# Optimization experiments

Hardware: AMD Instinct MI355X
Metric: run time of the kernel (lower is better)

## Reference

```python
import jax, jax.numpy as jnp
import numpy as np


def setup_inputs() -> dict:
    key = jax.random.key(0)
    ks = jax.random.split(key, 8)
    B, A = 2048, 64
    STATE, ACT = 5, 4
    d_in = STATE + ACT  # 9
    x = jax.random.normal(ks[0], (B, STATE), dtype=jnp.float32)
    actions = jax.random.normal(ks[1], (A, ACT), dtype=jnp.float32)
    def lin(k, fin, fout):
        return jax.random.normal(k, (fin, fout), dtype=jnp.float32) / np.sqrt(fin)
    W1 = lin(ks[2], d_in, 128); b1 = jnp.zeros((128,), jnp.float32)
    W2 = lin(ks[3], 128, 1024); b2 = jnp.zeros((1024,), jnp.float32)
    W3 = lin(ks[4], 1024, 1024); b3 = jnp.zeros((1024,), jnp.float32)
    W4 = lin(ks[5], 1024, 128); b4 = jnp.zeros((128,), jnp.float32)
    W5 = lin(ks[6], 128, 1); b5 = jnp.zeros((1,), jnp.float32)
    return {"x": x, "actions": actions,
            "W1": W1, "b1": b1, "W2": W2, "b2": b2, "W3": W3, "b3": b3,
            "W4": W4, "b4": b4, "W5": W5, "b5": b5}


def reference(x, actions, W1, b1, W2, b2, W3, b3, W4, b4, W5, b5):
    # x: [B,5] states; actions: [A,4] candidate actions.
    # Equivalent to the original's per-sample per-action loop: evaluate the
    # 5-layer Tanh MLP on concat(state, action) for every (sample, action) pair.
    B = x.shape[0]
    A = actions.shape[0]
    s = jnp.broadcast_to(x[:, None, :], (B, A, x.shape[1]))
    a = jnp.broadcast_to(actions[None, :, :], (B, A, actions.shape[1]))
    inp = jnp.concatenate([s, a], axis=-1)  # [B,A,9]
    h = jnp.tanh(inp @ W1 + b1)
    h = jnp.tanh(h @ W2 + b2)
    h = jnp.tanh(h @ W3 + b3)
    h = jnp.tanh(h @ W4 + b4)
    values = (h @ W5 + b5)[..., 0]  # [B,A]
    best = jnp.argmax(values, axis=1)  # [B]
    max_value_action = actions[best]  # [B,4]
    return (max_value_action, values)
```

## Files before the change

kernel.cpp:

```cpp
#include <hip/hip_runtime.h>
#include <math.h>


typedef short bf16x8 __attribute__((ext_vector_type(8)));
typedef float f32x4 __attribute__((ext_vector_type(4)));
typedef float f32x16 __attribute__((ext_vector_type(16)));

__device__ __host__ inline unsigned short f2bf(float f) {
    union { float f; unsigned u; } v; v.f = f;
    unsigned r = v.u + 0x7fff + ((v.u >> 16) & 1);
    return (unsigned short)(r >> 16);
}
__device__ inline float bf2f(unsigned short b) {
    union { unsigned u; float f; } v; v.u = ((unsigned)b) << 16;
    return v.f;
}
__device__ inline float fast_tanh(float x) {
    float e = __expf(2.0f * x);
    return 1.0f - 2.0f * __builtin_amdgcn_rcpf(e + 1.0f);
}

#define DELTA 0.025f
#define WL_CAP 4096

struct WLE { unsigned long long mask; unsigned s; unsigned pad; };

#define HSWZ(row, b) ((b) ^ (((row) & 15) << 4))

__global__ __launch_bounds__(256) void pack_w16(const float* __restrict__ src,
                                                unsigned short* __restrict__ dst,
                                                int K, int N) {
    int tid = blockIdx.x * 256 + threadIdx.x;
    int blob = tid >> 6, lane = tid & 63;
    int bpn = K >> 5;
    int nblob = (N >> 4) * bpn;
    if (blob >= nblob) return;
    int nt = blob / bpn, kt = blob % bpn;
    int n = nt * 16 + (lane & 15);
    int kbase = kt * 32 + ((lane >> 4) & 3) * 8;
    bf16x8 v;
    #pragma unroll
    for (int e = 0; e < 8; ++e) v[e] = (short)f2bf(src[(size_t)(kbase + e) * N + n]);
    *(bf16x8*)&dst[(size_t)blob * 512 + lane * 8] = v;
}
__global__ __launch_bounds__(256) void pack_w32(const float* __restrict__ src,
                                                unsigned short* __restrict__ dst,
                                                int K, int N) {
    int tid = blockIdx.x * 256 + threadIdx.x;
    int blob = tid >> 6, lane = tid & 63;
    int bpn = K >> 4;
    int nblob = (N >> 5) * bpn;
    if (blob >= nblob) return;
    int nt = blob / bpn, kt = blob % bpn;
    int n = nt * 32 + (lane & 31);
    int kbase = kt * 16 + (lane >> 5) * 8;
    bf16x8 v;
    #pragma unroll
    for (int e = 0; e < 8; ++e) v[e] = (short)f2bf(src[(size_t)(kbase + e) * N + n]);
    *(bf16x8*)&dst[(size_t)blob * 512 + lane * 8] = v;
}

__global__ __launch_bounds__(1024, 4) void qnet_mfma(
    const float* __restrict__ x, const float* __restrict__ actions,
    const float* __restrict__ W1, const float* __restrict__ b1,
    const float* __restrict__ b2, const float* __restrict__ b3,
    const float* __restrict__ b4,
    const float* __restrict__ W5, const float* __restrict__ b5,
    const unsigned short* __restrict__ W2p,
    const unsigned short* __restrict__ W3p,
    const unsigned short* __restrict__ W4p,
    float* __restrict__ values)
{
    __shared__ unsigned short h2[64 * 1024];
    __shared__ unsigned short hc[64 * 128];

    const int t = threadIdx.x;
    const int lane = t & 63;
    const int wave = t >> 6;
    const int p0 = blockIdx.x * 64;
    const int kb16 = (lane >> 4) * 16;
    const int kb32 = (lane >> 5) * 16;

    {
        int r = t >> 4;
        int c0 = (t & 15) * 8;
        const float* xs = &x[blockIdx.x * 5];
        const float* as = &actions[r * 4];
        float in[9] = { xs[0], xs[1], xs[2], xs[3], xs[4], as[0], as[1], as[2], as[3] };
        #pragma unroll
        for (int j = 0; j < 8; ++j) {
            int c = c0 + j;
            float acc = b1[c];
            #pragma unroll
            for (int k = 0; k < 9; ++k) acc += in[k] * W1[k * 128 + c];
            *(unsigned short*)((char*)hc + r * 256 + HSWZ(r, c * 2)) = f2bf(fast_tanh(acc));
        }
    }
    __syncthreads();

    {
        bf16x8 Af[4][4];
        #pragma unroll
        for (int rt = 0; rt < 4; ++rt)
            #pragma unroll
            for (int ks = 0; ks < 4; ++ks) {
                int row = rt * 16 + (lane & 15);
                Af[rt][ks] = *(const bf16x8*)((const char*)hc + row * 256 + HSWZ(row, ks * 64 + kb16));
            }
        #pragma unroll
        for (int j = 0; j < 4; ++j) {
            int nT = wave * 4 + j;
            float bv = b2[nT * 16 + (lane & 15)];
            f32x4 acc0 = (f32x4){ bv, bv, bv, bv };
            f32x4 acc1 = acc0, acc2 = acc0, acc3v = acc0;
            #pragma unroll
            for (int ks = 0; ks < 4; ++ks) {
                bf16x8 b = *(const bf16x8*)&W2p[((size_t)(nT * 4 + ks)) * 512 + lane * 8];
                acc0 = __builtin_amdgcn_mfma_f32_16x16x32_bf16(Af[0][ks], b, acc0, 0, 0, 0);
                acc1 = __builtin_amdgcn_mfma_f32_16x16x32_bf16(Af[1][ks], b, acc1, 0, 0, 0);
                acc2 = __builtin_amdgcn_mfma_f32_16x16x32_bf16(Af[2][ks], b, acc2, 0, 0, 0);
                acc3v = __builtin_amdgcn_mfma_f32_16x16x32_bf16(Af[3][ks], b, acc3v, 0, 0, 0);
            }
            int n = nT * 16 + (lane & 15);
            #pragma unroll
            for (int rr = 0; rr < 4; ++rr) {
                int m0 = (lane >> 4) * 4 + rr;
                *(unsigned short*)((char*)h2 + (m0 +  0) * 2048 + HSWZ(m0 +  0, n * 2)) = f2bf(fast_tanh(acc0[rr]));
                *(unsigned short*)((char*)h2 + (m0 + 16) * 2048 + HSWZ(m0 + 16, n * 2)) = f2bf(fast_tanh(acc1[rr]));
                *(unsigned short*)((char*)h2 + (m0 + 32) * 2048 + HSWZ(m0 + 32, n * 2)) = f2bf(fast_tanh(acc2[rr]));
                *(unsigned short*)((char*)h2 + (m0 + 48) * 2048 + HSWZ(m0 + 48, n * 2)) = f2bf(fast_tanh(acc3v[rr]));
            }
        }
    }
    __syncthreads();

    f32x16 a00, a01, a10, a11;
    {
        float bv0 = b3[wave * 64 + (lane & 31)];
        float bv1 = b3[wave * 64 + 32 + (lane & 31)];
        #pragma unroll
        for (int i = 0; i < 16; ++i) { a00[i] = bv0; a10[i] = bv0; a01[i] = bv1; a11[i] = bv1; }
    }
    const int r0 = lane & 31, r1 = 32 + (lane & 31);
    {
        const unsigned short* bbase = &W3p[((size_t)(wave * 2) * 64) * 512 + lane * 8];
        #pragma unroll 2
        for (int kt = 0; kt < 64; ++kt) {
            bf16x8 A0 = *(const bf16x8*)((const char*)h2 + r0 * 2048 + HSWZ(r0, kt * 32 + kb32));
            bf16x8 A1 = *(const bf16x8*)((const char*)h2 + r1 * 2048 + HSWZ(r1, kt * 32 + kb32));
            bf16x8 B0 = *(const bf16x8*)(bbase + (size_t)kt * 512);
            bf16x8 B1 = *(const bf16x8*)(bbase + (size_t)(64 + kt) * 512);
            a00 = __builtin_amdgcn_mfma_f32_32x32x16_bf16(A0, B0, a00, 0, 0, 0);
            a10 = __builtin_amdgcn_mfma_f32_32x32x16_bf16(A1, B0, a10, 0, 0, 0);
            a01 = __builtin_amdgcn_mfma_f32_32x32x16_bf16(A0, B1, a01, 0, 0, 0);
            a11 = __builtin_amdgcn_mfma_f32_32x32x16_bf16(A1, B1, a11, 0, 0, 0);
        }
    }
    __syncthreads();

    {
        int c0l = wave * 64 + (lane & 31);
        #pragma unroll
        for (int r = 0; r < 16; ++r) {
            int row = (r & 3) + 8 * (r >> 2) + 4 * (lane >> 5);
            int rowB = row + 32;
            *(unsigned short*)((char*)h2 + row  * 2048 + HSWZ(row,  c0l * 2)) = f2bf(fast_tanh(a00[r]));
            *(unsigned short*)((char*)h2 + rowB * 2048 + HSWZ(rowB, c0l * 2)) = f2bf(fast_tanh(a10[r]));
            *(unsigned short*)((char*)h2 + row  * 2048 + HSWZ(row,  (c0l + 32) * 2)) = f2bf(fast_tanh(a01[r]));
            *(unsigned short*)((char*)h2 + rowB * 2048 + HSWZ(rowB, (c0l + 32) * 2)) = f2bf(fast_tanh(a11[r]));
        }
    }
    __syncthreads();

    {
        const int ct = wave & 7, rtp = wave >> 3;
        const int rowA = rtp * 32 + (lane & 15);
        const int rowB = rowA + 16;
        float bv = b4[ct * 16 + (lane & 15)];
        f32x4 acc4a = (f32x4){ bv, bv, bv, bv };
        f32x4 acc4b = acc4a;
        #pragma unroll 4
        for (int k32 = 0; k32 < 32; ++k32) {
            bf16x8 B = *(const bf16x8*)&W4p[((size_t)(ct * 32 + k32)) * 512 + lane * 8];
            bf16x8 aA = *(const bf16x8*)((const char*)h2 + rowA * 2048 + HSWZ(rowA, k32 * 64 + kb16));
            bf16x8 aB = *(const bf16x8*)((const char*)h2 + rowB * 2048 + HSWZ(rowB, k32 * 64 + kb16));
            acc4a = __builtin_amdgcn_mfma_f32_16x16x32_bf16(aA, B, acc4a, 0, 0, 0);
            acc4b = __builtin_amdgcn_mfma_f32_16x16x32_bf16(aB, B, acc4b, 0, 0, 0);
        }
        int n = ct * 16 + (lane & 15);
        #pragma unroll
        for (int rr = 0; rr < 4; ++rr) {
            int mA = rtp * 32 + (lane >> 4) * 4 + rr;
            int mB = mA + 16;
            *(unsigned short*)((char*)hc + mA * 256 + HSWZ(mA, n * 2)) = f2bf(fast_tanh(acc4a[rr]));
            *(unsigned short*)((char*)hc + mB * 256 + HSWZ(mB, n * 2)) = f2bf(fast_tanh(acc4b[rr]));
        }
    }
    __syncthreads();

    {
        int r = t >> 4, g = t & 15;
        float part = 0.0f;
        #pragma unroll
        for (int j = 0; j < 8; ++j) {
            int cidx = g * 8 + j;
            unsigned short hb = *(const unsigned short*)((const char*)hc + r * 256 + HSWZ(r, cidx * 2));
            part += bf2f(hb) * W5[cidx];
        }
        part += __shfl_down(part, 8);
        part += __shfl_down(part, 4);
        part += __shfl_down(part, 2);
        part += __shfl_down(part, 1);
        if (g == 0) values[p0 + r] = part + b5[0];
    }
}

__global__ void wl_init(unsigned* wl_cnt) {
    if (threadIdx.x == 0 && blockIdx.x == 0) *wl_cnt = 0u;
}

__global__ __launch_bounds__(256) void scan_argmax(
    const float* __restrict__ values, const float* __restrict__ actions,
    float* __restrict__ out_actions, unsigned* __restrict__ wl_cnt,
    WLE* __restrict__ wl)
{
    int wave = threadIdx.x >> 6, lane = threadIdx.x & 63;
    int s = blockIdx.x * 4 + wave;
    float myv = values[s * 64 + lane];
    float v = myv; int idx = lane;
    #pragma unroll
    for (int off = 32; off; off >>= 1) {
        float ov = __shfl_down(v, off);
        int oi = __shfl_down(idx, off);
        if (ov > v || (ov == v && oi < idx)) { v = ov; idx = oi; }
    }
    float vm = __shfl(v, 0);
    int best = __shfl(idx, 0);
    unsigned long long mask = __ballot(myv >= vm - DELTA);
    if (lane == 0 && __popcll(mask) > 1) {
        unsigned slot = atomicAdd(wl_cnt, 1u);
        if (slot < WL_CAP) { wl[slot].mask = mask; wl[slot].s = (unsigned)s; }
    }
    if (lane < 4) out_actions[s * 4 + lane] = actions[best * 4 + lane];
}

__global__ __launch_bounds__(256) void fixup_eval(
    const float* __restrict__ x, const float* __restrict__ actions,
    const float* __restrict__ W1, const float* __restrict__ b1,
    const float* __restrict__ W2, const float* __restrict__ b2,
    const float* __restrict__ W3, const float* __restrict__ b3,
    const float* __restrict__ W4, const float* __restrict__ b4,
    const float* __restrict__ W5, const float* __restrict__ b5,
    const unsigned* __restrict__ wl_cnt, const WLE* __restrict__ wl,
    float* __restrict__ out_actions)
{
    __shared__ float h1s[8][128];
    __shared__ float h2s[8][1024];
    __shared__ float h3s[8][1024];
    __shared__ float h4s[8][128];
    __shared__ float ain[8][4];
    __shared__ float xs[5];
    __shared__ int cand[64];
    __shared__ int ncand;
    __shared__ float vals[8];
    __shared__ float bestv; __shared__ int besti;

    const int t = threadIdx.x;
    int n = (int)*wl_cnt;
    if (n > WL_CAP) n = WL_CAP;
    for (int e = blockIdx.x; e < n; e += gridDim.x) {
        unsigned long long mask = wl[e].mask;
        int s = (int)wl[e].s;
        if (t == 0) {
            int nn = 0; unsigned long long m2 = mask;
            while (m2) { cand[nn++] = __ffsll(m2) - 1; m2 &= m2 - 1; }
            ncand = nn; bestv = -1e30f; besti = 0;
        }
        if (t < 5) xs[t] = x[s * 5 + t];
        __syncthreads();
        const int NC = ncand;
        for (int g = 0; g < NC; g += 8) {
            if (t < 32) {
                int rr = t >> 2;
                int src = (g + rr < NC) ? cand[g + rr] : cand[g];
                ain[rr][t & 3] = actions[src * 4 + (t & 3)];
            }
            __syncthreads();
            {
                int r = t >> 5, cb = (t & 31) * 4;
                #pragma unroll
                for (int j = 0; j < 4; ++j) {
                    int c = cb + j;
                    float acc = b1[c];
                    #pragma unroll
                    for (int k = 0; k < 5; ++k) acc += xs[k] * W1[k * 128 + c];
                    #pragma unroll
                    for (int k = 0; k < 4; ++k) acc += ain[r][k] * W1[(5 + k) * 128 + c];
                    h1s[r][c] = tanhf(acc);
                }
            }
            __syncthreads();
            {
                int cb = t * 4;
                float acc[8][4];
                float4 bv = *(const float4*)&b2[cb];
                #pragma unroll
                for (int r = 0; r < 8; ++r) { acc[r][0]=bv.x; acc[r][1]=bv.y; acc[r][2]=bv.z; acc[r][3]=bv.w; }
                for (int k = 0; k < 128; ++k) {
                    float4 w = *(const float4*)&W2[k * 1024 + cb];
                    #pragma unroll
                    for (int r = 0; r < 8; ++r) {
                        float hv = h1s[r][k];
                        acc[r][0] += hv * w.x; acc[r][1] += hv * w.y;
                        acc[r][2] += hv * w.z; acc[r][3] += hv * w.w;
                    }
                }
                #pragma unroll
                for (int r = 0; r < 8; ++r) {
                    h2s[r][cb+0] = tanhf(acc[r][0]); h2s[r][cb+1] = tanhf(acc[r][1]);
                    h2s[r][cb+2] = tanhf(acc[r][2]); h2s[r][cb+3] = tanhf(acc[r][3]);
                }
            }
            __syncthreads();
            {
                int cb = t * 4;
                float acc[8][4];
                float4 bv = *(const float4*)&b3[cb];
                #pragma unroll
                for (int r = 0; r < 8; ++r) { acc[r][0]=bv.x; acc[r][1]=bv.y; acc[r][2]=bv.z; acc[r][3]=bv.w; }
                for (int k = 0; k < 1024; ++k) {
                    float4 w = *(const float4*)&W3[k * 1024 + cb];
                    #pragma unroll
                    for (int r = 0; r < 8; ++r) {
                        float hv = h2s[r][k];
                        acc[r][0] += hv * w.x; acc[r][1] += hv * w.y;
                        acc[r][2] += hv * w.z; acc[r][3] += hv * w.w;
                    }
                }
                #pragma unroll
                for (int r = 0; r < 8; ++r) {
                    h3s[r][cb+0] = tanhf(acc[r][0]); h3s[r][cb+1] = tanhf(acc[r][1]);
                    h3s[r][cb+2] = tanhf(acc[r][2]); h3s[r][cb+3] = tanhf(acc[r][3]);
                }
            }
            __syncthreads();
            {
                int r = t >> 5, cb = (t & 31) * 4;
                float acc[4];
                float4 bv = *(const float4*)&b4[cb];
                acc[0]=bv.x; acc[1]=bv.y; acc[2]=bv.z; acc[3]=bv.w;
                for (int k = 0; k < 1024; ++k) {
                    float4 w = *(const float4*)&W4[k * 128 + cb];
                    float hv = h3s[r][k];
                    acc[0] += hv * w.x; acc[1] += hv * w.y; acc[2] += hv * w.z; acc[3] += hv * w.w;
                }
                h4s[r][cb+0] = tanhf(acc[0]); h4s[r][cb+1] = tanhf(acc[1]);
                h4s[r][cb+2] = tanhf(acc[2]); h4s[r][cb+3] = tanhf(acc[3]);
            }
            __syncthreads();
            if (t < 8) {
                float acc = b5[0];
                for (int k = 0; k < 128; ++k) acc += h4s[t][k] * W5[k];
                vals[t] = acc;
            }
            __syncthreads();
            if (t == 0) {
                int lim = (NC - g < 8) ? (NC - g) : 8;
                for (int i = 0; i < lim; ++i)
                    if (vals[i] > bestv) { bestv = vals[i]; besti = cand[g + i]; }
            }
            __syncthreads();
        }
        if (t < 4) out_actions[s * 4 + t] = actions[besti * 4 + t];
        __syncthreads();
    }
}

#define TR 16
__global__ __launch_bounds__(256) void qnet_fused(
    const float* __restrict__ x, const float* __restrict__ actions,
    const float* __restrict__ W1, const float* __restrict__ b1,
    const float* __restrict__ W2, const float* __restrict__ b2,
    const float* __restrict__ W3, const float* __restrict__ b3,
    const float* __restrict__ W4, const float* __restrict__ b4,
    const float* __restrict__ W5, const float* __restrict__ b5,
    float* __restrict__ values)
{
    __shared__ float h_small[TR][128];
    __shared__ float hA[TR][1024];
    __shared__ float hB[TR][1024];
    const int t = threadIdx.x;
    const int p0 = blockIdx.x * TR;
    for (int i = t; i < TR * 128; i += 256) {
        int r = i >> 7, c = i & 127;
        int p = p0 + r;
        int bidx = p >> 6, aidx = p & 63;
        float acc = b1[c];
        for (int k = 0; k < 5; ++k) acc += x[bidx * 5 + k] * W1[k * 128 + c];
        for (int k = 0; k < 4; ++k) acc += actions[aidx * 4 + k] * W1[(5 + k) * 128 + c];
        h_small[r][c] = tanhf(acc);
    }
    __syncthreads();
    {
        const int c0 = t * 4;
        float4 bias = *(const float4*)&b2[c0];
        float acc[TR][4];
        for (int r = 0; r < TR; ++r) { acc[r][0]=bias.x; acc[r][1]=bias.y; acc[r][2]=bias.z; acc[r][3]=bias.w; }
        for (int k = 0; k < 128; k += 4) {
            float4 w0 = *(const float4*)&W2[(k+0)*1024+c0];
            float4 w1 = *(const float4*)&W2[(k+1)*1024+c0];
            float4 w2 = *(const float4*)&W2[(k+2)*1024+c0];
            float4 w3 = *(const float4*)&W2[(k+3)*1024+c0];
            for (int r = 0; r < TR; ++r) {
                float4 hv = *(const float4*)&h_small[r][k];
                acc[r][0] += hv.x*w0.x + hv.y*w1.x + hv.z*w2.x + hv.w*w3.x;
                acc[r][1] += hv.x*w0.y + hv.y*w1.y + hv.z*w2.y + hv.w*w3.y;
                acc[r][2] += hv.x*w0.z + hv.y*w1.z + hv.z*w2.z + hv.w*w3.z;
                acc[r][3] += hv.x*w0.w + hv.y*w1.w + hv.z*w2.w + hv.w*w3.w;
            }
        }
        for (int r = 0; r < TR; ++r) {
            hA[r][c0+0]=tanhf(acc[r][0]); hA[r][c0+1]=tanhf(acc[r][1]);
            hA[r][c0+2]=tanhf(acc[r][2]); hA[r][c0+3]=tanhf(acc[r][3]);
        }
    }
    __syncthreads();
    {
        const int c0 = t * 4;
        float4 bias = *(const float4*)&b3[c0];
        float acc[TR][4];
        for (int r = 0; r < TR; ++r) { acc[r][0]=bias.x; acc[r][1]=bias.y; acc[r][2]=bias.z; acc[r][3]=bias.w; }
        for (int k = 0; k < 1024; k += 4) {
            float4 w0 = *(const float4*)&W3[(k+0)*1024+c0];
            float4 w1 = *(const float4*)&W3[(k+1)*1024+c0];
            float4 w2 = *(const float4*)&W3[(k+2)*1024+c0];
            float4 w3 = *(const float4*)&W3[(k+3)*1024+c0];
            for (int r = 0; r < TR; ++r) {
                float4 hv = *(const float4*)&hA[r][k];
                acc[r][0] += hv.x*w0.x + hv.y*w1.x + hv.z*w2.x + hv.w*w3.x;
                acc[r][1] += hv.x*w0.y + hv.y*w1.y + hv.z*w2.y + hv.w*w3.y;
                acc[r][2] += hv.x*w0.z + hv.y*w1.z + hv.z*w2.z + hv.w*w3.z;
                acc[r][3] += hv.x*w0.w + hv.y*w1.w + hv.z*w2.w + hv.w*w3.w;
            }
        }
        for (int r = 0; r < TR; ++r) {
            hB[r][c0+0]=tanhf(acc[r][0]); hB[r][c0+1]=tanhf(acc[r][1]);
            hB[r][c0+2]=tanhf(acc[r][2]); hB[r][c0+3]=tanhf(acc[r][3]);
        }
    }
    __syncthreads();
    {
        const int c = t & 127;
        const int rh = t >> 7;
        float acc[8];
        float bias = b4[c];
        for (int r = 0; r < 8; ++r) acc[r] = bias;
        for (int k = 0; k < 1024; k += 4) {
            float w0 = W4[(k+0)*128+c], w1 = W4[(k+1)*128+c];
            float w2 = W4[(k+2)*128+c], w3 = W4[(k+3)*128+c];
            for (int r = 0; r < 8; ++r) {
                float4 hv = *(const float4*)&hB[rh*8+r][k];
                acc[r] += hv.x*w0 + hv.y*w1 + hv.z*w2 + hv.w*w3;
            }
        }
        for (int r = 0; r < 8; ++r) h_small[rh*8+r][c] = tanhf(acc[r]);
    }
    __syncthreads();
    if (t < TR) {
        float acc = b5[0];
        for (int k = 0; k < 128; k += 4) {
            float4 hv = *(const float4*)&h_small[t][k];
            float4 wv = *(const float4*)&W5[k];
            acc += hv.x*wv.x + hv.y*wv.y + hv.z*wv.z + hv.w*wv.w;
        }
        values[p0 + t] = acc;
    }
}

__global__ __launch_bounds__(256) void argmax_gather(
    const float* __restrict__ values, const float* __restrict__ actions,
    float* __restrict__ out_actions)
{
    const int wave = threadIdx.x >> 6;
    const int lane = threadIdx.x & 63;
    const int state = blockIdx.x * (blockDim.x >> 6) + wave;
    float v = values[state * 64 + lane];
    int idx = lane;
    for (int off = 32; off; off >>= 1) {
        float ov = __shfl_down(v, off);
        int oi = __shfl_down(idx, off);
        if (ov > v || (ov == v && oi < idx)) { v = ov; idx = oi; }
    }
    idx = __shfl(idx, 0);
    if (lane < 4) out_actions[state * 4 + lane] = actions[idx * 4 + lane];
}

extern "C" void kernel_launch(void* const* d_in, const int* in_sizes, int n_in,
                              void* d_out, int out_size, void* d_ws, size_t ws_size,
                              hipStream_t stream) {
    const float* x       = (const float*)d_in[0];
    const float* actions = (const float*)d_in[1];
    const float* W1 = (const float*)d_in[2];  const float* b1 = (const float*)d_in[3];
    const float* W2 = (const float*)d_in[4];  const float* b2 = (const float*)d_in[5];
    const float* W3 = (const float*)d_in[6];  const float* b3 = (const float*)d_in[7];
    const float* W4 = (const float*)d_in[8];  const float* b4 = (const float*)d_in[9];
    const float* W5 = (const float*)d_in[10]; const float* b5 = (const float*)d_in[11];

    float* out_actions = (float*)d_out;
    float* values      = (float*)d_out + 2048 * 4;

    const size_t nW2 = 128 * 1024, nW3 = 1024 * 1024, nW4 = 1024 * 128;
    const size_t wbytes = (nW2 + nW3 + nW4) * sizeof(unsigned short);
    const size_t need = wbytes + 16 + (size_t)WL_CAP * sizeof(WLE);

    if (ws_size >= need) {
        unsigned short* W2p = (unsigned short*)d_ws;
        unsigned short* W3p = W2p + nW2;
        unsigned short* W4p = W3p + nW3;
        unsigned* wl_cnt = (unsigned*)((char*)d_ws + wbytes);
        WLE* wl = (WLE*)((char*)d_ws + wbytes + 16);

        pack_w16<<<(int)((nW2 / 8 + 255) / 256), 256, 0, stream>>>(W2, W2p, 128, 1024);
        pack_w32<<<(int)((nW3 / 8 + 255) / 256), 256, 0, stream>>>(W3, W3p, 1024, 1024);
        pack_w16<<<(int)((nW4 / 8 + 255) / 256), 256, 0, stream>>>(W4, W4p, 1024, 128);
        wl_init<<<1, 64, 0, stream>>>(wl_cnt);
        qnet_mfma<<<2048, 1024, 0, stream>>>(x, actions, W1, b1, b2, b3, b4, W5, b5,
                                             W2p, W3p, W4p, values);
        scan_argmax<<<512, 256, 0, stream>>>(values, actions, out_actions, wl_cnt, wl);
        fixup_eval<<<512, 256, 0, stream>>>(x, actions, W1, b1, W2, b2, W3, b3,
                                            W4, b4, W5, b5, wl_cnt, wl, out_actions);
    } else {
        qnet_fused<<<2048 * 64 / TR, 256, 0, stream>>>(x, actions, W1, b1, W2, b2, W3, b3,
                                                       W4, b4, W5, b5, values);
        argmax_gather<<<2048 / 4, 256, 0, stream>>>(values, actions, out_actions);
    }
}
```

Measured before the change: 626.4 us.

## Chunk layer-2 into double-buffered LDS stages and merge weight-packing launches

```diff
diff --git a/kernel.cpp b/kernel.cpp
--- a/kernel.cpp
+++ b/kernel.cpp
@@ -27,37 +27,40 @@
 
 #define HSWZ(row, b) ((b) ^ (((row) & 15) << 4))
 
-__global__ __launch_bounds__(256) void pack_w16(const float* __restrict__ src,
-                                                unsigned short* __restrict__ dst,
-                                                int K, int N) {
+__global__ __launch_bounds__(256) void pack_all(
+    const float* __restrict__ W2, const float* __restrict__ W3, const float* __restrict__ W4,
+    unsigned short* __restrict__ W2p, unsigned short* __restrict__ W3p,
+    unsigned short* __restrict__ W4p, unsigned* __restrict__ wl_cnt)
+{
     int tid = blockIdx.x * 256 + threadIdx.x;
+    if (tid == 0) *wl_cnt = 0u;
     int blob = tid >> 6, lane = tid & 63;
-    int bpn = K >> 5;
-    int nblob = (N >> 4) * bpn;
-    if (blob >= nblob) return;
-    int nt = blob / bpn, kt = blob % bpn;
-    int n = nt * 16 + (lane & 15);
-    int kbase = kt * 32 + ((lane >> 4) & 3) * 8;
+    if (blob >= 2560) return;
     bf16x8 v;
-    #pragma unroll
-    for (int e = 0; e < 8; ++e) v[e] = (short)f2bf(src[(size_t)(kbase + e) * N + n]);
-    *(bf16x8*)&dst[(size_t)blob * 512 + lane * 8] = v;
-}
-__global__ __launch_bounds__(256) void pack_w32(const float* __restrict__ src,
-                                                unsigned short* __restrict__ dst,
-                                                int K, int N) {
-    int tid = blockIdx.x * 256 + threadIdx.x;
-    int blob = tid >> 6, lane = tid & 63;
-    int bpn = K >> 4;
-    int nblob = (N >> 5) * bpn;
-    if (blob >= nblob) return;
-    int nt = blob / bpn, kt = blob % bpn;
-    int n = nt * 32 + (lane & 31);
-    int kbase = kt * 16 + (lane >> 5) * 8;
-    bf16x8 v;
-    #pragma unroll
-    for (int e = 0; e < 8; ++e) v[e] = (short)f2bf(src[(size_t)(kbase + e) * N + n]);
-    *(bf16x8*)&dst[(size_t)blob * 512 + lane * 8] = v;
+    if (blob < 256) {
+        int nt = blob >> 2, kt = blob & 3;
+        int n = nt * 16 + (lane & 15);
+        int kbase = kt * 32 + ((lane >> 4) & 3) * 8;
+        #pragma unroll
+        for (int e = 0; e < 8; ++e) v[e] = (short)f2bf(W2[(size_t)(kbase + e) * 1024 + n]);
+        *(bf16x8*)&W2p[(size_t)blob * 512 + lane * 8] = v;
+    } else if (blob < 2304) {
+        int lb = blob - 256;
+        int nt = lb >> 6, kt = lb & 63;
+        int n = nt * 32 + (lane & 31);
+        int kbase = kt * 16 + (lane >> 5) * 8;
+        #pragma unroll
+        for (int e = 0; e < 8; ++e) v[e] = (short)f2bf(W3[(size_t)(kbase + e) * 1024 + n]);
+        *(bf16x8*)&W3p[(size_t)lb * 512 + lane * 8] = v;
+    } else {
+        int lb = blob - 2304;
+        int nt = lb >> 5, kt = lb & 31;
+        int n = nt * 16 + (lane & 15);
+        int kbase = kt * 32 + ((lane >> 4) & 3) * 8;
+        #pragma unroll
+        for (int e = 0; e < 8; ++e) v[e] = (short)f2bf(W4[(size_t)(kbase + e) * 128 + n]);
+        *(bf16x8*)&W4p[(size_t)lb * 512 + lane * 8] = v;
+    }
 }
 
 __global__ __launch_bounds__(1024, 4) void qnet_mfma(
@@ -71,7 +74,7 @@
     const unsigned short* __restrict__ W4p,
     float* __restrict__ values)
 {
-    __shared__ unsigned short h2[64 * 1024];
+    __shared__ unsigned short h2b[2][64 * 256];
     __shared__ unsigned short hc[64 * 128];
 
     const int t = threadIdx.x;
@@ -98,41 +101,34 @@
     }
     __syncthreads();
 
-    {
-        bf16x8 Af[4][4];
-        #pragma unroll
-        for (int rt = 0; rt < 4; ++rt)
-            #pragma unroll
-            for (int ks = 0; ks < 4; ++ks) {
-                int row = rt * 16 + (lane & 15);
-                Af[rt][ks] = *(const bf16x8*)((const char*)hc + row * 256 + HSWZ(row, ks * 64 + kb16));
-            }
-        #pragma unroll
-        for (int j = 0; j < 4; ++j) {
-            int nT = wave * 4 + j;
-            float bv = b2[nT * 16 + (lane & 15)];
-            f32x4 acc0 = (f32x4){ bv, bv, bv, bv };
-            f32x4 acc1 = acc0, acc2 = acc0, acc3v = acc0;
-            #pragma unroll
-            for (int ks = 0; ks < 4; ++ks) {
-                bf16x8 b = *(const bf16x8*)&W2p[((size_t)(nT * 4 + ks)) * 512 + lane * 8];
-                acc0 = __builtin_amdgcn_mfma_f32_16x16x32_bf16(Af[0][ks], b, acc0, 0, 0, 0);
-                acc1 = __builtin_amdgcn_mfma_f32_16x16x32_bf16(Af[1][ks], b, acc1, 0, 0, 0);
-                acc2 = __builtin_amdgcn_mfma_f32_16x16x32_bf16(Af[2][ks], b, acc2, 0, 0, 0);
-                acc3v = __builtin_amdgcn_mfma_f32_16x16x32_bf16(Af[3][ks], b, acc3v, 0, 0, 0);
-            }
-            int n = nT * 16 + (lane & 15);
-            #pragma unroll
-            for (int rr = 0; rr < 4; ++rr) {
-                int m0 = (lane >> 4) * 4 + rr;
-                *(unsigned short*)((char*)h2 + (m0 +  0) * 2048 + HSWZ(m0 +  0, n * 2)) = f2bf(fast_tanh(acc0[rr]));
-                *(unsigned short*)((char*)h2 + (m0 + 16) * 2048 + HSWZ(m0 + 16, n * 2)) = f2bf(fast_tanh(acc1[rr]));
-                *(unsigned short*)((char*)h2 + (m0 + 32) * 2048 + HSWZ(m0 + 32, n * 2)) = f2bf(fast_tanh(acc2[rr]));
-                *(unsigned short*)((char*)h2 + (m0 + 48) * 2048 + HSWZ(m0 + 48, n * 2)) = f2bf(fast_tanh(acc3v[rr]));
-            }
-        }
-    }
-    __syncthreads();
+    auto layer2_chunk = [&](int c, int buf) {
+        int nT = c * 16 + wave;
+        float bv = b2[nT * 16 + (lane & 15)];
+        f32x4 acc0 = (f32x4){ bv, bv, bv, bv };
+        f32x4 acc1 = acc0, acc2 = acc0, acc3v = acc0;
+        #pragma unroll
+        for (int ks = 0; ks < 4; ++ks) {
+            bf16x8 b = *(const bf16x8*)&W2p[((size_t)(nT * 4 + ks)) * 512 + lane * 8];
+            bf16x8 a0 = *(const bf16x8*)((const char*)hc + ( 0 + (lane & 15)) * 256 + HSWZ((lane & 15),      ks * 64 + kb16));
+            bf16x8 a1 = *(const bf16x8*)((const char*)hc + (16 + (lane & 15)) * 256 + HSWZ(16 + (lane & 15), ks * 64 + kb16));
+            bf16x8 a2 = *(const bf16x8*)((const char*)hc + (32 + (lane & 15)) * 256 + HSWZ(32 + (lane & 15), ks * 64 + kb16));
+            bf16x8 a3 = *(const bf16x8*)((const char*)hc + (48 + (lane & 15)) * 256 + HSWZ(48 + (lane & 15), ks * 64 + kb16));
+            acc0 = __builtin_amdgcn_mfma_f32_16x16x32_bf16(a0, b, acc0, 0, 0, 0);
+            acc1 = __builtin_amdgcn_mfma_f32_16x16x32_bf16(a1, b, acc1, 0, 0, 0);
+            acc2 = __builtin_amdgcn_mfma_f32_16x16x32_bf16(a2, b, acc2, 0, 0, 0);
+            acc3v = __builtin_amdgcn_mfma_f32_16x16x32_bf16(a3, b, acc3v, 0, 0, 0);
+        }
+        int lc = wave * 16 + (lane & 15);
+        char* bufp = (char*)&h2b[buf][0];
+        #pragma unroll
+        for (int rr = 0; rr < 4; ++rr) {
+            int m0 = (lane >> 4) * 4 + rr;
+            *(unsigned short*)(bufp + (m0 +  0) * 512 + HSWZ(m0 +  0, lc * 2)) = f2bf(fast_tanh(acc0[rr]));
+            *(unsigned short*)(bufp + (m0 + 16) * 512 + HSWZ(m0 + 16, lc * 2)) = f2bf(fast_tanh(acc1[rr]));
+            *(unsigned short*)(bufp + (m0 + 32) * 512 + HSWZ(m0 + 32, lc * 2)) = f2bf(fast_tanh(acc2[rr]));
+            *(unsigned short*)(bufp + (m0 + 48) * 512 + HSWZ(m0 + 48, lc * 2)) = f2bf(fast_tanh(acc3v[rr]));
+        }
+    };
 
     f32x16 a00, a01, a10, a11;
     {
@@ -141,62 +137,61 @@
         #pragma unroll
         for (int i = 0; i < 16; ++i) { a00[i] = bv0; a10[i] = bv0; a01[i] = bv1; a11[i] = bv1; }
     }
+
+    layer2_chunk(0, 0);
+    __syncthreads();
+
     const int r0 = lane & 31, r1 = 32 + (lane & 31);
-    {
-        const unsigned short* bbase = &W3p[((size_t)(wave * 2) * 64) * 512 + lane * 8];
+    for (int c = 0; c < 4; ++c) {
+        if (c < 3) layer2_chunk(c + 1, (c + 1) & 1);
+        const char* buf = (const char*)&h2b[c & 1][0];
+        const unsigned short* bb = &W3p[((size_t)((wave * 2) * 64 + c * 16)) * 512 + lane * 8];
         #pragma unroll 2
-        for (int kt = 0; kt < 64; ++kt) {
-            bf16x8 A0 = *(const bf16x8*)((const char*)h2 + r0 * 2048 + HSWZ(r0, kt * 32 + kb32));
-            bf16x8 A1 = *(const bf16x8*)((const char*)h2 + r1 * 2048 + HSWZ(r1, kt * 32 + kb32));
-            bf16x8 B0 = *(const bf16x8*)(bbase + (size_t)kt * 512);
-            bf16x8 B1 = *(const bf16x8*)(bbase + (size_t)(64 + kt) * 512);
+        for (int kt = 0; kt < 16; ++kt) {
+            bf16x8 A0 = *(const bf16x8*)(buf + r0 * 512 + HSWZ(r0, kt * 32 + kb32));
+            bf16x8 A1 = *(const bf16x8*)(buf + r1 * 512 + HSWZ(r1, kt * 32 + kb32));
+            bf16x8 B0 = *(const bf16x8*)(bb + (size_t)kt * 512);
+            bf16x8 B1 = *(const bf16x8*)(bb + (size_t)(64 + kt) * 512);
             a00 = __builtin_amdgcn_mfma_f32_32x32x16_bf16(A0, B0, a00, 0, 0, 0);
             a10 = __builtin_amdgcn_mfma_f32_32x32x16_bf16(A1, B0, a10, 0, 0, 0);
             a01 = __builtin_amdgcn_mfma_f32_32x32x16_bf16(A0, B1, a01, 0, 0, 0);
             a11 = __builtin_amdgcn_mfma_f32_32x32x16_bf16(A1, B1, a11, 0, 0, 0);
         }
-    }
-    __syncthreads();
-
-    {
-        int c0l = wave * 64 + (lane & 31);
+        __syncthreads();
+    }
+
+    char* stage = (char*)&h2b[0][0];
+    const int ct = wave & 7, rtp = wave >> 3;
+    const int c0l = wave * 64 + (lane & 31);
+    const float bv4 = b4[ct * 16 + (lane & 15)];
+
+    #pragma unroll
+    for (int h = 0; h < 2; ++h) {
         #pragma unroll
         for (int r = 0; r < 16; ++r) {
             int row = (r & 3) + 8 * (r >> 2) + 4 * (lane >> 5);
-            int rowB = row + 32;
-            *(unsigned short*)((char*)h2 + row  * 2048 + HSWZ(row,  c0l * 2)) = f2bf(fast_tanh(a00[r]));
-            *(unsigned short*)((char*)h2 + rowB * 2048 + HSWZ(rowB, c0l * 2)) = f2bf(fast_tanh(a10[r]));
-            *(unsigned short*)((char*)h2 + row  * 2048 + HSWZ(row,  (c0l + 32) * 2)) = f2bf(fast_tanh(a01[r]));
-            *(unsigned short*)((char*)h2 + rowB * 2048 + HSWZ(rowB, (c0l + 32) * 2)) = f2bf(fast_tanh(a11[r]));
-        }
-    }
-    __syncthreads();
-
-    {
-        const int ct = wave & 7, rtp = wave >> 3;
-        const int rowA = rtp * 32 + (lane & 15);
-        const int rowB = rowA + 16;
-        float bv = b4[ct * 16 + (lane & 15)];
-        f32x4 acc4a = (f32x4){ bv, bv, bv, bv };
-        f32x4 acc4b = acc4a;
+            float vlo = h ? a10[r] : a00[r];
+            float vhi = h ? a11[r] : a01[r];
+            *(unsigned short*)(stage + row * 2048 + HSWZ(row, c0l * 2)) = f2bf(fast_tanh(vlo));
+            *(unsigned short*)(stage + row * 2048 + HSWZ(row, (c0l + 32) * 2)) = f2bf(fast_tanh(vhi));
+        }
+        __syncthreads();
+        f32x4 acc4 = (f32x4){ bv4, bv4, bv4, bv4 };
+        const int rowL = rtp * 16 + (lane & 15);
         #pragma unroll 4
         for (int k32 = 0; k32 < 32; ++k32) {
             bf16x8 B = *(const bf16x8*)&W4p[((size_t)(ct * 32 + k32)) * 512 + lane * 8];
-            bf16x8 aA = *(const bf16x8*)((const char*)h2 + rowA * 2048 + HSWZ(rowA, k32 * 64 + kb16));
-            bf16x8 aB = *(const bf16x8*)((const char*)h2 + rowB * 2048 + HSWZ(rowB, k32 * 64 + kb16));
-            acc4a = __builtin_amdgcn_mfma_f32_16x16x32_bf16(aA, B, acc4a, 0, 0, 0);
-            acc4b = __builtin_amdgcn_mfma_f32_16x16x32_bf16(aB, B, acc4b, 0, 0, 0);
+            bf16x8 a = *(const bf16x8*)(stage + rowL * 2048 + HSWZ(rowL, k32 * 64 + kb16));
+            acc4 = __builtin_amdgcn_mfma_f32_16x16x32_bf16(a, B, acc4, 0, 0, 0);
         }
         int n = ct * 16 + (lane & 15);
         #pragma unroll
         for (int rr = 0; rr < 4; ++rr) {
-            int mA = rtp * 32 + (lane >> 4) * 4 + rr;
-            int mB = mA + 16;
-            *(unsigned short*)((char*)hc + mA * 256 + HSWZ(mA, n * 2)) = f2bf(fast_tanh(acc4a[rr]));
-            *(unsigned short*)((char*)hc + mB * 256 + HSWZ(mB, n * 2)) = f2bf(fast_tanh(acc4b[rr]));
-        }
-    }
-    __syncthreads();
+            int m = h * 32 + rtp * 16 + (lane >> 4) * 4 + rr;
+            *(unsigned short*)((char*)hc + m * 256 + HSWZ(m, n * 2)) = f2bf(fast_tanh(acc4[rr]));
+        }
+        __syncthreads();
+    }
 
     {
         int r = t >> 4, g = t & 15;
@@ -213,10 +208,6 @@
         part += __shfl_down(part, 1);
         if (g == 0) values[p0 + r] = part + b5[0];
     }
-}
-
-__global__ void wl_init(unsigned* wl_cnt) {
-    if (threadIdx.x == 0 && blockIdx.x == 0) *wl_cnt = 0u;
 }
 
 __global__ __launch_bounds__(256) void scan_argmax(
@@ -520,10 +511,7 @@
         unsigned* wl_cnt = (unsigned*)((char*)d_ws + wbytes);
         WLE* wl = (WLE*)((char*)d_ws + wbytes + 16);
 
-        pack_w16<<<(int)((nW2 / 8 + 255) / 256), 256, 0, stream>>>(W2, W2p, 128, 1024);
-        pack_w32<<<(int)((nW3 / 8 + 255) / 256), 256, 0, stream>>>(W3, W3p, 1024, 1024);
-        pack_w16<<<(int)((nW4 / 8 + 255) / 256), 256, 0, stream>>>(W4, W4p, 1024, 128);
-        wl_init<<<1, 64, 0, stream>>>(wl_cnt);
+        pack_all<<<640, 256, 0, stream>>>(W2, W3, W4, W2p, W3p, W4p, wl_cnt);
         qnet_mfma<<<2048, 1024, 0, stream>>>(x, actions, W1, b1, b2, b3, b4, W5, b5,
                                              W2p, W3p, W4p, values);
         scan_argmax<<<512, 256, 0, stream>>>(values, actions, out_actions, wl_cnt, wl);
```

After: 744.3 us. +18.8%, slower.
